# Kernel tuning notes

Measured on AMD Instinct MI355X. Metric: run time of the kernel, lower is better.

The kernel has to match this reference:

```python
import jax, jax.numpy as jnp
import numpy as np

EMBED_DIM = 768
NUM_HEADS = 12
HEAD_DIM = EMBED_DIM // NUM_HEADS
EPS = 1e-5  # nn.LayerNorm default


def setup_inputs() -> dict:
    key = jax.random.key(0)
    ks = jax.random.split(key, 7)
    D = EMBED_DIM
    s1 = 1.0 / np.sqrt(D)
    x = jax.random.normal(ks[0], (2, 2048, D), dtype=jnp.float32)
    # LayerNorm params
    gamma = jnp.ones((D,), jnp.float32)
    beta = jnp.zeros((D,), jnp.float32)
    # QKV projection (linear1): weight [3D, D], bias [3D]
    w1 = jax.random.uniform(ks[1], (3 * D, D), jnp.float32, -s1, s1)
    b1 = jax.random.uniform(ks[2], (3 * D,), jnp.float32, -s1, s1)
    # Output projection (linear2[0]): weight [D, D], bias [D]
    w2 = jax.random.uniform(ks[3], (D, D), jnp.float32, -s1, s1)
    b2 = jax.random.uniform(ks[4], (D,), jnp.float32, -s1, s1)
    return {"x": x, "gamma": gamma, "beta": beta, "w1": w1, "b1": b1, "w2": w2, "b2": b2}


def _layernorm(x, gamma, beta):
    mu = jnp.mean(x, axis=-1, keepdims=True)
    var = jnp.mean(jnp.square(x - mu), axis=-1, keepdims=True)
    return (x - mu) * jax.lax.rsqrt(var + EPS) * gamma + beta


def reference(x, gamma, beta, w1, b1, w2, b2) -> jnp.ndarray:
    B, L, D = x.shape
    H, Dh = NUM_HEADS, HEAD_DIM
    residual = x
    h = _layernorm(x, gamma, beta)
    qkv = h @ w1.T + b1  # [B, L, 3D]
    q, k, v = jnp.split(qkv, 3, axis=-1)
    # 'b n (h d) -> b h n d'
    q = q.reshape(B, L, H, Dh).transpose(0, 2, 1, 3)
    k = k.reshape(B, L, H, Dh).transpose(0, 2, 1, 3)
    v = v.reshape(B, L, H, Dh).transpose(0, 2, 1, 3)
    scores = jnp.einsum("bhqd,bhkd->bhqk", q, k) / jnp.sqrt(jnp.float32(Dh))
    attn = jax.nn.softmax(scores, axis=-1)  # dropout is identity in eval mode
    out = jnp.einsum("bhqk,bhkd->bhqd", attn, v)  # [B, H, L, Dh]
    out = out.transpose(0, 2, 1, 3).reshape(B, L, D)
    out = out @ w2.T + b2  # dropout identity in eval
    return residual + out
```

## Files before the change

kernel.cpp:

```cpp
#include <hip/hip_runtime.h>


#define DEV __device__ __forceinline__

typedef __attribute__((ext_vector_type(4))) float f32x4;
typedef __attribute__((ext_vector_type(8))) short s16x8;
typedef __attribute__((ext_vector_type(2))) int i32x2;

constexpr int Bb   = 2;
constexpr int Ll   = 2048;
constexpr int Dd   = 768;
constexpr int Hh   = 12;
constexpr int Dh   = 64;
constexpr int Mrows = Bb * Ll;
constexpr int N1   = 3 * Dd;

DEV unsigned short f2bf(float f) {
  union { float f; unsigned u; } v; v.f = f;
  unsigned r = v.u + 0x7fffu + ((v.u >> 16) & 1u);
  return (unsigned short)(r >> 16);
}

DEV void gload_lds16(const void* g, void* l) {
  __builtin_amdgcn_global_load_lds((const __attribute__((address_space(1))) unsigned int*)g,
                                   (__attribute__((address_space(3))) unsigned int*)l,
                                   16, 0, 0);
}

DEV f32x4 mfma16(s16x8 a, s16x8 b, f32x4 c) {
  return __builtin_amdgcn_mfma_f32_16x16x32_bf16(a, b, c, 0, 0, 0);
}

DEV float fexp2(float x) { float r; asm("v_exp_f32 %0, %1" : "=v"(r) : "v"(x)); return r; }
DEV float frcp(float x)  { float r; asm("v_rcp_f32 %0, %1" : "=v"(r) : "v"(x)); return r; }

DEV float redmax64(float x) {
  x = fmaxf(x, __shfl_xor(x, 16, 64));
  float a = x, b = x;
  asm volatile("v_permlane32_swap_b32 %0, %1" : "+v"(a), "+v"(b));
  return fmaxf(a, b);
}
DEV float redsum64(float x) {
  x += __shfl_xor(x, 16, 64);
  float a = x, b = x;
  asm volatile("v_permlane32_swap_b32 %0, %1" : "+v"(a), "+v"(b));
  return a + b;
}

DEV void ln_body(int row, int t, const float* __restrict__ x,
                 const float* __restrict__ gamma, const float* __restrict__ beta,
                 short* __restrict__ hbuf, float* red) {
  const float* xr = x + (size_t)row * Dd;
  float v0 = xr[t], v1 = xr[t + 256], v2 = xr[t + 512];
  float s = v0 + v1 + v2;
  float q = v0 * v0 + v1 * v1 + v2 * v2;
#pragma unroll
  for (int off = 32; off; off >>= 1) {
    s += __shfl_xor(s, off, 64);
    q += __shfl_xor(q, off, 64);
  }
  const int w = t >> 6, lane = t & 63;
  if (lane == 0) { red[w] = s; red[4 + w] = q; }
  __syncthreads();
  s = red[0] + red[1] + red[2] + red[3];
  q = red[4] + red[5] + red[6] + red[7];
  const float mean = s * (1.f / Dd);
  const float var  = q * (1.f / Dd) - mean * mean;
  const float rstd = rsqrtf(var + 1e-5f);
  short* hr = hbuf + (size_t)row * Dd;
  hr[t]       = (short)f2bf((v0 - mean) * rstd * gamma[t]       + beta[t]);
  hr[t + 256] = (short)f2bf((v1 - mean) * rstd * gamma[t + 256] + beta[t + 256]);
  hr[t + 512] = (short)f2bf((v2 - mean) * rstd * gamma[t + 512] + beta[t + 512]);
}

constexpr int W1E = N1 * Dd;
constexpr int W2E = Dd * Dd;

__global__ __launch_bounds__(256) void ln_kernel(const float* __restrict__ x,
                                                 const float* __restrict__ gamma,
                                                 const float* __restrict__ beta,
                                                 short* __restrict__ hbuf) {
  __shared__ float red[8];
  ln_body(blockIdx.x, threadIdx.x, x, gamma, beta, hbuf, red);
}

__global__ __launch_bounds__(256) void cvt_kernel(const float* __restrict__ w1,
                                                  const float* __restrict__ w2,
                                                  short* __restrict__ w1b,
                                                  short* __restrict__ w2b) {
  int i = blockIdx.x * 256 + threadIdx.x;
  const int stride = gridDim.x * 256;
  for (; i < W1E + W2E; i += stride) {
    if (i < W1E) w1b[i] = (short)f2bf(w1[i]);
    else         w2b[i - W1E] = (short)f2bf(w2[i - W1E]);
  }
}

__global__ __launch_bounds__(256) void prep_kernel(const float* __restrict__ x,
                                                   const float* __restrict__ gamma,
                                                   const float* __restrict__ beta,
                                                   short* __restrict__ hbuf,
                                                   const float* __restrict__ w1,
                                                   const float* __restrict__ w2,
                                                   short* __restrict__ w1b,
                                                   short* __restrict__ w2b) {
  __shared__ float red[8];
  if (blockIdx.x < (unsigned)Mrows) {
    ln_body(blockIdx.x, threadIdx.x, x, gamma, beta, hbuf, red);
  } else {
    int i = (blockIdx.x - Mrows) * 256 + threadIdx.x;
    for (; i < W1E + W2E; i += 1024 * 256) {
      if (i < W1E) w1b[i] = (short)f2bf(w1[i]);
      else         w2b[i - W1E] = (short)f2bf(w2[i - W1E]);
    }
  }
}

DEV unsigned xcd_swz(unsigned f, unsigned nwg) {
  if ((nwg & 7u) != 0u) return f;
  return (f & 7u) * (nwg >> 3) + (f >> 3);
}

template <int EPI, int WSRC>
__global__ __launch_bounds__(256) void gemm_bt(const short* __restrict__ A,
                                               const void* __restrict__ Wp,
                                               const float* __restrict__ bias,
                                               const float* __restrict__ resid,
                                               void* __restrict__ outp,
                                               int N, int K) {
  __shared__ __align__(16) short As[2][128 * 64];
  __shared__ __align__(16) short Ws[2][128 * 64];
  const int tid  = threadIdx.x;
  const int lane = tid & 63, wid = tid >> 6;
  const int wr = wid >> 1, wc = wid & 1;
  const int g = lane >> 4, li = lane & 15;
  const unsigned o = xcd_swz(blockIdx.y * gridDim.x + blockIdx.x,
                             gridDim.x * gridDim.y);
  const int brow = (int)(o / gridDim.x) * 128, bcol = (int)(o % gridDim.x) * 128;

  f32x4 acc[4][4];
#pragma unroll
  for (int m = 0; m < 4; ++m)
#pragma unroll
    for (int n = 0; n < 4; ++n)
#pragma unroll
      for (int r = 0; r < 4; ++r) acc[m][n][r] = 0.f;

  if constexpr (WSRC == 0) {
    const short* W = (const short*)Wp;
    const int nt = K >> 6;
    auto stage = [&](int t, int buf) {
      const int ko = t << 6;
#pragma unroll
      for (int i = 0; i < 4; ++i) {
        const int idx = i * 256 + tid;
        const int r = idx >> 3, c = idx & 7;
        const int cs = c ^ (r & 7);
        gload_lds16(A + (size_t)(brow + r) * K + ko + cs * 8,
                    (char*)&As[buf][0] + idx * 16);
        gload_lds16(W + (size_t)(bcol + r) * K + ko + cs * 8,
                    (char*)&Ws[buf][0] + idx * 16);
      }
    };
    stage(0, 0);
    stage(1, 1);
    for (int it = 0; it < nt; ++it) {
      const int cur = it & 1;
      if (it + 1 < nt) asm volatile("s_waitcnt vmcnt(8)" ::: "memory");
      else             asm volatile("s_waitcnt vmcnt(0)" ::: "memory");
      __builtin_amdgcn_s_barrier();
      __builtin_amdgcn_sched_barrier(0);
#pragma unroll
      for (int kk = 0; kk < 2; ++kk) {
        s16x8 af[4], bf[4];
#pragma unroll
        for (int m = 0; m < 4; ++m) {
          const int row = wr * 64 + m * 16 + li;
          af[m] = *(const s16x8*)&As[cur][row * 64 + (((kk * 4 + g) ^ (li & 7)) & 7) * 8];
        }
#pragma unroll
        for (int n = 0; n < 4; ++n) {
          const int row = wc * 64 + n * 16 + li;
          bf[n] = *(const s16x8*)&Ws[cur][row * 64 + (((kk * 4 + g) ^ (li & 7)) & 7) * 8];
        }
#pragma unroll
        for (int m = 0; m < 4; ++m)
#pragma unroll
          for (int n = 0; n < 4; ++n)
            acc[m][n] = mfma16(af[m], bf[n], acc[m][n]);
      }
      __builtin_amdgcn_s_barrier();
      if (it + 2 < nt) stage(it + 2, cur);
    }
  } else {
    const float* W = (const float*)Wp;
    for (int kt = 0; kt < K; kt += 64) {
#pragma unroll
      for (int i = 0; i < 4; ++i) {
        const int idx = i * 256 + tid;
        const int r = idx >> 3, c = idx & 7;
        const int cs = c ^ (r & 7);
        gload_lds16(A + (size_t)(brow + r) * K + kt + cs * 8,
                    (char*)&As[0][0] + idx * 16);
      }
#pragma unroll
      for (int i = 0; i < 4; ++i) {
        const int idx = i * 256 + tid;
        const int r = idx >> 3, c = idx & 7;
        const float* wp = W + (size_t)(bcol + r) * K + kt + c * 8;
        const f32x4 lo = *(const f32x4*)wp;
        const f32x4 hi = *(const f32x4*)(wp + 4);
        s16x8 oo;
#pragma unroll
        for (int j = 0; j < 4; ++j) {
          oo[j]     = (short)f2bf(lo[j]);
          oo[4 + j] = (short)f2bf(hi[j]);
        }
        *(s16x8*)((char*)&Ws[0][0] + (size_t)(r * 8 + (c ^ (r & 7))) * 16) = oo;
      }
      __syncthreads();
#pragma unroll
      for (int kk = 0; kk < 2; ++kk) {
        s16x8 af[4], bf[4];
#pragma unroll
        for (int m = 0; m < 4; ++m) {
          const int row = wr * 64 + m * 16 + li;
          af[m] = *(const s16x8*)&As[0][row * 64 + (((kk * 4 + g) ^ (li & 7)) & 7) * 8];
        }
#pragma unroll
        for (int n = 0; n < 4; ++n) {
          const int row = wc * 64 + n * 16 + li;
          bf[n] = *(const s16x8*)&Ws[0][row * 64 + (((kk * 4 + g) ^ (li & 7)) & 7) * 8];
        }
#pragma unroll
        for (int m = 0; m < 4; ++m)
#pragma unroll
          for (int n = 0; n < 4; ++n)
            acc[m][n] = mfma16(af[m], bf[n], acc[m][n]);
      }
      __syncthreads();
    }
  }

#pragma unroll
  for (int m = 0; m < 4; ++m) {
#pragma unroll
    for (int n = 0; n < 4; ++n) {
      const int col = bcol + wc * 64 + n * 16 + li;
      const float bv = bias[col];
#pragma unroll
      for (int r = 0; r < 4; ++r) {
        const int row = brow + wr * 64 + m * 16 + g * 4 + r;
        const float v = acc[m][n][r] + bv;
        if (EPI == 0) {
          ((short*)outp)[(size_t)row * N + col] = (short)f2bf(v);
        } else {
          const size_t o2 = (size_t)row * N + col;
          ((float*)outp)[o2] = v + resid[o2];
        }
      }
    }
  }
}

#define TRRD(dst, addr, OFF)                                                   \
  asm volatile("ds_read_b64_tr_b16 %0, %1 offset:" #OFF                        \
               : "=v"(dst) : "v"(addr))

__global__ __launch_bounds__(256) void attn_kernel(const short* __restrict__ qkv,
                                                   short* __restrict__ obuf) {
  __shared__ __align__(16) short Ks[2][64 * 64];
  __shared__ __align__(16) short Vt[2][64 * 64];
  __shared__ __align__(16) short Ps[4][16 * 64];
  const int tid  = threadIdx.x;
  const int lane = tid & 63, w = tid >> 6;
  const int g = lane >> 4, li = lane & 15;
  const unsigned o = xcd_swz(blockIdx.y * 32u + blockIdx.x, gridDim.x * gridDim.y);
  const int bh = (int)(o >> 5);
  const int b = bh / Hh, h = bh % Hh;
  const size_t rowbase = (size_t)b * Ll * N1;
  const int q0 = (int)(o & 31u) * 64 + w * 16;
  constexpr float kScale = 0.125f * 1.44269504f;
  constexpr float kThrRaw = 8.f / kScale;
  constexpr int KVSTRIDE = 64 * N1;

  s16x8 qf[2];
#pragma unroll
  for (int ks = 0; ks < 2; ++ks)
    qf[ks] = *(const s16x8*)(qkv + rowbase + (size_t)(q0 + li) * N1 +
                             h * Dh + ks * 32 + g * 8);

  f32x4 oa[4];
  float m_ = -1e30f, l_ = 0.f;
#pragma unroll
  for (int dn = 0; dn < 4; ++dn)
#pragma unroll
    for (int r = 0; r < 4; ++r) oa[dn][r] = 0.f;

  constexpr int NT = Ll / 64;

  const int ia = tid, ib = 256 + tid;
  const int ra = ia >> 3, ca = ia & 7, rb = ib >> 3, cb = ib & 7;
  const short* kpa = qkv + rowbase + Dd + h * Dh + (size_t)ra * N1 + (ca ^ (ra & 7)) * 8;
  const short* kpb = qkv + rowbase + Dd + h * Dh + (size_t)rb * N1 + (cb ^ (rb & 7)) * 8;
  const int Ta = ia >> 3, Tb = ib >> 3;
  const short* vpa = qkv + rowbase + 2 * Dd + h * Dh +
                     (size_t)((Ta & 15) * 4 + (ca >> 1)) * N1 + (Ta >> 4) * 16 + (ia & 1) * 8;
  const short* vpb = qkv + rowbase + 2 * Dd + h * Dh +
                     (size_t)((Tb & 15) * 4 + (cb >> 1)) * N1 + (Tb >> 4) * 16 + (ib & 1) * 8;
  char* KsB = (char*)&Ks[0][0];
  char* VtB = (char*)&Vt[0][0];
  const int dsta = ia * 16, dstb = ib * 16;

  int koff[4][2];
#pragma unroll
  for (int n = 0; n < 4; ++n) {
    koff[n][0] = ((n * 16 + li) * 64 + ((g ^ (li & 7)) & 7) * 8) * 2;
    koff[n][1] = ((n * 16 + li) * 64 + (((4 + g) ^ (li & 7)) & 7) * 8) * 2;
  }
  int pwoff[4], proff[2];
#pragma unroll
  for (int n = 0; n < 4; ++n)
    pwoff[n] = li * 128 + (((2 * n + (g >> 1)) ^ (li & 7)) << 4) + 8 * (g & 1);
#pragma unroll
  for (int kk = 0; kk < 2; ++kk)
    proff[kk] = li * 128 + (((4 * kk + g) ^ (li & 7)) << 4);
  char* Pw = (char*)&Ps[w][0];
  const unsigned vlane = (unsigned)((lane >> 4) * 256 + (lane & 15) * 2);
  const unsigned vbase0 = (unsigned)(unsigned long long)(&Vt[0][0]) + vlane;

  auto stageK = [&](int buf) {
    const int bo = buf << 13;
    gload_lds16(kpa, KsB + bo + dsta);
    gload_lds16(kpb, KsB + bo + dstb);
    kpa += KVSTRIDE; kpb += KVSTRIDE;
  };
  auto stageV = [&](int buf) {
    const int bo = buf << 13;
    gload_lds16(vpa, VtB + bo + dsta);
    gload_lds16(vpb, VtB + bo + dstb);
    vpa += KVSTRIDE; vpb += KVSTRIDE;
  };

  stageK(0); stageV(0); stageK(1); stageV(1);
  asm volatile("s_waitcnt vmcnt(4)" ::: "memory");
  __builtin_amdgcn_s_barrier();
  __builtin_amdgcn_sched_barrier(0);

  f32x4 zA[4], zB[4];
#pragma unroll
  for (int n = 0; n < 4; ++n) {
    s16x8 kf0 = *(const s16x8*)(KsB + koff[n][0]);
    s16x8 kf1 = *(const s16x8*)(KsB + koff[n][1]);
    f32x4 z;
#pragma unroll
    for (int r = 0; r < 4; ++r) z[r] = 0.f;
    z = mfma16(kf0, qf[0], z);
    z = mfma16(kf1, qf[1], z);
    zA[n] = z;
  }

  for (int kt = 0; kt < NT; ++kt) {
    const int cur = kt & 1;
    const int curo = cur << 13;
    const int nxto = (cur ^ 1) << 13;
    if (kt + 1 < NT) asm volatile("s_waitcnt vmcnt(2)" ::: "memory");
    else             asm volatile("s_waitcnt vmcnt(0)" ::: "memory");
    __builtin_amdgcn_s_barrier();
    __builtin_amdgcn_sched_barrier(0);

    if (kt + 2 < NT) stageK(cur);

    if (kt + 1 < NT) {
      __builtin_amdgcn_s_setprio(1);
#pragma unroll
      for (int n = 0; n < 4; ++n) {
        s16x8 kf0 = *(const s16x8*)(KsB + nxto + koff[n][0]);
        s16x8 kf1 = *(const s16x8*)(KsB + nxto + koff[n][1]);
        f32x4 z;
#pragma unroll
        for (int r = 0; r < 4; ++r) z[r] = 0.f;
        z = mfma16(kf0, qf[0], z);
        z = mfma16(kf1, qf[1], z);
        zB[n] = z;
      }
      __builtin_amdgcn_s_setprio(0);
    }

    const float l0 = fmaxf(fmaxf(zA[0][0], zA[0][1]), zA[0][2]);
    const float l1 = fmaxf(fmaxf(zA[0][3], zA[1][0]), zA[1][1]);
    const float l2 = fmaxf(fmaxf(zA[1][2], zA[1][3]), zA[2][0]);
    const float l3 = fmaxf(fmaxf(zA[2][1], zA[2][2]), zA[2][3]);
    const float l4 = fmaxf(fmaxf(zA[3][0], zA[3][1]), zA[3][2]);
    float mx = fmaxf(fmaxf(fmaxf(fmaxf(l0, l1), l2), fmaxf(l3, l4)), zA[3][3]);
    mx = redmax64(mx);
    if (!__all(mx - m_ <= kThrRaw)) {
      const float mnew = fmaxf(m_, mx);
      const float sc = fexp2((m_ - mnew) * kScale);
      float scq[4];
#pragma unroll
      for (int r = 0; r < 4; ++r)
        scq[r] = __shfl(sc, (lane & 48) + ((lane & 48) >> 2) + r, 64);
#pragma unroll
      for (int dn = 0; dn < 4; ++dn)
#pragma unroll
        for (int r = 0; r < 4; ++r) oa[dn][r] *= scq[r];
      l_ *= sc;
      m_ = mnew;
    }
    const float msc = m_ * kScale;
    float rs = 0.f;
#pragma unroll
    for (int n = 0; n < 4; ++n)
#pragma unroll
      for (int r = 0; r < 4; ++r) {
        const float p = fexp2(fmaf(zA[n][r], kScale, -msc));
        zA[n][r] = p;
        rs += p;
      }
    rs = redsum64(rs);
    l_ += rs;

#pragma unroll
    for (int n = 0; n < 4; ++n) {
      unsigned u0, u1;
      asm("v_cvt_pk_bf16_f32 %0, %1, %2" : "=v"(u0) : "v"(zA[n][0]), "v"(zA[n][1]));
      asm("v_cvt_pk_bf16_f32 %0, %1, %2" : "=v"(u1) : "v"(zA[n][2]), "v"(zA[n][3]));
      i32x2 pv; pv[0] = (int)u0; pv[1] = (int)u1;
      *(i32x2*)(Pw + pwoff[n]) = pv;
    }

    s16x8 pf[2];
#pragma unroll
    for (int kk = 0; kk < 2; ++kk)
      pf[kk] = *(const s16x8*)(Pw + proff[kk]);

    union VU { long l[2]; s16x8 v; };
    VU vu[4][2];
    {
      const unsigned vaddr = vbase0 + (unsigned)curo;
      TRRD(vu[0][0].l[0], vaddr, 0);    TRRD(vu[0][0].l[1], vaddr, 128);
      TRRD(vu[0][1].l[0], vaddr, 1024); TRRD(vu[0][1].l[1], vaddr, 1152);
      TRRD(vu[1][0].l[0], vaddr, 2048); TRRD(vu[1][0].l[1], vaddr, 2176);
      TRRD(vu[1][1].l[0], vaddr, 3072); TRRD(vu[1][1].l[1], vaddr, 3200);
      TRRD(vu[2][0].l[0], vaddr, 4096); TRRD(vu[2][0].l[1], vaddr, 4224);
      TRRD(vu[2][1].l[0], vaddr, 5120); TRRD(vu[2][1].l[1], vaddr, 5248);
      TRRD(vu[3][0].l[0], vaddr, 6144); TRRD(vu[3][0].l[1], vaddr, 6272);
      TRRD(vu[3][1].l[0], vaddr, 7168); TRRD(vu[3][1].l[1], vaddr, 7296);
    }
    asm volatile("s_waitcnt lgkmcnt(0)" ::: "memory");
    __builtin_amdgcn_sched_barrier(0);

    __builtin_amdgcn_s_setprio(1);
#pragma unroll
    for (int dn = 0; dn < 4; ++dn) {
      oa[dn] = mfma16(pf[0], vu[dn][0].v, oa[dn]);
      oa[dn] = mfma16(pf[1], vu[dn][1].v, oa[dn]);
    }
    __builtin_amdgcn_s_setprio(0);

    __builtin_amdgcn_s_barrier();
    if (kt + 2 < NT) stageV(cur);
    if (kt + 1 < NT) {
#pragma unroll
      for (int n = 0; n < 4; ++n) zA[n] = zB[n];
    }
  }

  {
#pragma unroll
    for (int r = 0; r < 4; ++r) {
      const float lq = __shfl(l_, (lane & 48) + ((lane & 48) >> 2) + r, 64);
      const float inv = frcp(lq);
      const int row = b * Ll + q0 + g * 4 + r;
#pragma unroll
      for (int dn = 0; dn < 4; ++dn)
        obuf[(size_t)row * Dd + h * Dh + dn * 16 + li] =
            (short)f2bf(oa[dn][r] * inv);
    }
  }
}

extern "C" void kernel_launch(void* const* d_in, const int* in_sizes, int n_in,
                              void* d_out, int out_size, void* d_ws, size_t ws_size,
                              hipStream_t stream) {
  const float* x     = (const float*)d_in[0];
  const float* gamma = (const float*)d_in[1];
  const float* beta  = (const float*)d_in[2];
  const float* w1    = (const float*)d_in[3];
  const float* b1    = (const float*)d_in[4];
  const float* w2    = (const float*)d_in[5];
  const float* b2    = (const float*)d_in[6];
  float* out = (float*)d_out;
  char* ws = (char*)d_ws;

  if (ws_size >= 29884416) {
    short* qkvb = (short*)(ws);
    short* hb   = (short*)(ws + 18874368);
    short* w1b  = (short*)(ws + 25165824);
    short* w2b  = (short*)(ws + 28704768);
    prep_kernel<<<dim3(Mrows + 1024), dim3(256), 0, stream>>>(
        x, gamma, beta, hb, w1, w2, w1b, w2b);
    gemm_bt<0, 0><<<dim3(N1 / 128, Mrows / 128), dim3(256), 0, stream>>>(
        hb, w1b, b1, nullptr, (void*)qkvb, N1, Dd);
    attn_kernel<<<dim3(Ll / 64, Bb * Hh), dim3(256), 0, stream>>>(qkvb, hb);
    gemm_bt<1, 0><<<dim3(Dd / 128, Mrows / 128), dim3(256), 0, stream>>>(
        hb, w2b, b2, x, (void*)out, Dd, Dd);
  } else if (ws_size >= 17301504) {
    short* qkvb = (short*)(ws);
    short* hb   = (short*)(ws + 9437184);
    short* w1b  = (short*)(ws + 12582912);
    short* w2b  = (short*)(ws + 16121856);
    cvt_kernel<<<dim3(1024), dim3(256), 0, stream>>>(w1, w2, w1b, w2b);
    for (int b = 0; b < Bb; ++b) {
      const size_t ro = (size_t)b * Ll * Dd;
      ln_kernel<<<dim3(Ll), dim3(256), 0, stream>>>(x + ro, gamma, beta, hb);
      gemm_bt<0, 0><<<dim3(N1 / 128, Ll / 128), dim3(256), 0, stream>>>(
          hb, w1b, b1, nullptr, (void*)qkvb, N1, Dd);
      attn_kernel<<<dim3(Ll / 64, Hh), dim3(256), 0, stream>>>(qkvb, hb);
      gemm_bt<1, 0><<<dim3(Dd / 128, Ll / 128), dim3(256), 0, stream>>>(
          hb, w2b, b2, x + ro, (void*)(out + ro), Dd, Dd);
    }
  } else {
    short* qkvb = (short*)(ws);
    short* hb   = (short*)(ws + 9437184);
    for (int b = 0; b < Bb; ++b) {
      const size_t ro = (size_t)b * Ll * Dd;
      ln_kernel<<<dim3(Ll), dim3(256), 0, stream>>>(x + ro, gamma, beta, hb);
      gemm_bt<0, 1><<<dim3(N1 / 128, Ll / 128), dim3(256), 0, stream>>>(
          hb, w1, b1, nullptr, (void*)qkvb, N1, Dd);
      attn_kernel<<<dim3(Ll / 64, Hh), dim3(256), 0, stream>>>(qkvb, hb);
      gemm_bt<1, 1><<<dim3(Dd / 128, Ll / 128), dim3(256), 0, stream>>>(
          hb, w2, b2, x + ro, (void*)(out + ro), Dd, Dd);
    }
  }
}
```

Measured before the change: 114.2 us.

## Rewrite attention with 32x32 MFMA, register-resident P and split-KV wave pairs

The attention kernel now uses 32x32x16 bf16 MFMAs. Each wave handles 32 query rows, and the two wave pairs each process half of the KV sequence (16 tiles each), with a final LDS merge of the partial softmax states. P is converted and rearranged in registers with permlane32 swaps instead of a round-trip through LDS. The old double-buffered K/V prefetch pipeline and the early QK^T overlap are dropped in favour of a simple load, wait and compute loop per tile, which risks exposing global load latency.

Result: slower. 122.2 us (+7.0%).

```diff
diff --git a/kernel.cpp b/kernel.cpp
--- a/kernel.cpp
+++ b/kernel.cpp
@@ -4,6 +4,7 @@
 #define DEV __device__ __forceinline__
 
 typedef __attribute__((ext_vector_type(4))) float f32x4;
+typedef __attribute__((ext_vector_type(16))) float f32x16;
 typedef __attribute__((ext_vector_type(8))) short s16x8;
 typedef __attribute__((ext_vector_type(2))) int i32x2;
 
@@ -30,22 +31,12 @@
 DEV f32x4 mfma16(s16x8 a, s16x8 b, f32x4 c) {
   return __builtin_amdgcn_mfma_f32_16x16x32_bf16(a, b, c, 0, 0, 0);
 }
+DEV f32x16 mfma32(s16x8 a, s16x8 b, f32x16 c) {
+  return __builtin_amdgcn_mfma_f32_32x32x16_bf16(a, b, c, 0, 0, 0);
+}
 
 DEV float fexp2(float x) { float r; asm("v_exp_f32 %0, %1" : "=v"(r) : "v"(x)); return r; }
 DEV float frcp(float x)  { float r; asm("v_rcp_f32 %0, %1" : "=v"(r) : "v"(x)); return r; }
-
-DEV float redmax64(float x) {
-  x = fmaxf(x, __shfl_xor(x, 16, 64));
-  float a = x, b = x;
-  asm volatile("v_permlane32_swap_b32 %0, %1" : "+v"(a), "+v"(b));
-  return fmaxf(a, b);
-}
-DEV float redsum64(float x) {
-  x += __shfl_xor(x, 16, 64);
-  float a = x, b = x;
-  asm volatile("v_permlane32_swap_b32 %0, %1" : "+v"(a), "+v"(b));
-  return a + b;
-}
 
 DEV void ln_body(int row, int t, const float* __restrict__ x,
                  const float* __restrict__ gamma, const float* __restrict__ beta,
@@ -271,213 +262,207 @@
                                                    short* __restrict__ obuf) {
   __shared__ __align__(16) short Ks[2][64 * 64];
   __shared__ __align__(16) short Vt[2][64 * 64];
-  __shared__ __align__(16) short Ps[4][16 * 64];
   const int tid  = threadIdx.x;
   const int lane = tid & 63, w = tid >> 6;
-  const int g = lane >> 4, li = lane & 15;
+  const int pair = w >> 1, qh = w & 1;
+  const int l5 = lane >> 5, lq = lane & 31;
   const unsigned o = xcd_swz(blockIdx.y * 32u + blockIdx.x, gridDim.x * gridDim.y);
   const int bh = (int)(o >> 5);
   const int b = bh / Hh, h = bh % Hh;
   const size_t rowbase = (size_t)b * Ll * N1;
-  const int q0 = (int)(o & 31u) * 64 + w * 16;
+  const int q0 = (int)(o & 31u) * 64 + qh * 32;
   constexpr float kScale = 0.125f * 1.44269504f;
   constexpr float kThrRaw = 8.f / kScale;
-  constexpr int KVSTRIDE = 64 * N1;
-
-  s16x8 qf[2];
-#pragma unroll
-  for (int ks = 0; ks < 2; ++ks)
-    qf[ks] = *(const s16x8*)(qkv + rowbase + (size_t)(q0 + li) * N1 +
-                             h * Dh + ks * 32 + g * 8);
-
-  f32x4 oa[4];
+  constexpr int KVS = 64 * N1;
+  constexpr int NT = 16;
+
+  s16x8 qf[4];
+#pragma unroll
+  for (int mf = 0; mf < 4; ++mf)
+    qf[mf] = *(const s16x8*)(qkv + rowbase + (size_t)(q0 + lq) * N1 +
+                             h * Dh + mf * 16 + l5 * 8);
+
+  f32x16 oa[2];
+#pragma unroll
+  for (int rt = 0; rt < 2; ++rt)
+#pragma unroll
+    for (int i = 0; i < 16; ++i) oa[rt][i] = 0.f;
   float m_ = -1e30f, l_ = 0.f;
-#pragma unroll
-  for (int dn = 0; dn < 4; ++dn)
-#pragma unroll
-    for (int r = 0; r < 4; ++r) oa[dn][r] = 0.f;
-
-  constexpr int NT = Ll / 64;
-
-  const int ia = tid, ib = 256 + tid;
-  const int ra = ia >> 3, ca = ia & 7, rb = ib >> 3, cb = ib & 7;
-  const short* kpa = qkv + rowbase + Dd + h * Dh + (size_t)ra * N1 + (ca ^ (ra & 7)) * 8;
-  const short* kpb = qkv + rowbase + Dd + h * Dh + (size_t)rb * N1 + (cb ^ (rb & 7)) * 8;
-  const int Ta = ia >> 3, Tb = ib >> 3;
-  const short* vpa = qkv + rowbase + 2 * Dd + h * Dh +
-                     (size_t)((Ta & 15) * 4 + (ca >> 1)) * N1 + (Ta >> 4) * 16 + (ia & 1) * 8;
-  const short* vpb = qkv + rowbase + 2 * Dd + h * Dh +
-                     (size_t)((Tb & 15) * 4 + (cb >> 1)) * N1 + (Tb >> 4) * 16 + (ib & 1) * 8;
-  char* KsB = (char*)&Ks[0][0];
-  char* VtB = (char*)&Vt[0][0];
-  const int dsta = ia * 16, dstb = ib * 16;
-
-  int koff[4][2];
-#pragma unroll
-  for (int n = 0; n < 4; ++n) {
-    koff[n][0] = ((n * 16 + li) * 64 + ((g ^ (li & 7)) & 7) * 8) * 2;
-    koff[n][1] = ((n * 16 + li) * 64 + (((4 + g) ^ (li & 7)) & 7) * 8) * 2;
-  }
-  int pwoff[4], proff[2];
-#pragma unroll
-  for (int n = 0; n < 4; ++n)
-    pwoff[n] = li * 128 + (((2 * n + (g >> 1)) ^ (li & 7)) << 4) + 8 * (g & 1);
-#pragma unroll
-  for (int kk = 0; kk < 2; ++kk)
-    proff[kk] = li * 128 + (((4 * kk + g) ^ (li & 7)) << 4);
-  char* Pw = (char*)&Ps[w][0];
-  const unsigned vlane = (unsigned)((lane >> 4) * 256 + (lane & 15) * 2);
-  const unsigned vbase0 = (unsigned)(unsigned long long)(&Vt[0][0]) + vlane;
-
-  auto stageK = [&](int buf) {
-    const int bo = buf << 13;
-    gload_lds16(kpa, KsB + bo + dsta);
-    gload_lds16(kpb, KsB + bo + dstb);
-    kpa += KVSTRIDE; kpb += KVSTRIDE;
-  };
-  auto stageV = [&](int buf) {
-    const int bo = buf << 13;
-    gload_lds16(vpa, VtB + bo + dsta);
-    gload_lds16(vpb, VtB + bo + dstb);
-    vpa += KVSTRIDE; vpb += KVSTRIDE;
-  };
-
-  stageK(0); stageV(0); stageK(1); stageV(1);
-  asm volatile("s_waitcnt vmcnt(4)" ::: "memory");
-  __builtin_amdgcn_s_barrier();
-  __builtin_amdgcn_sched_barrier(0);
-
-  f32x4 zA[4], zB[4];
-#pragma unroll
-  for (int n = 0; n < 4; ++n) {
-    s16x8 kf0 = *(const s16x8*)(KsB + koff[n][0]);
-    s16x8 kf1 = *(const s16x8*)(KsB + koff[n][1]);
-    f32x4 z;
-#pragma unroll
-    for (int r = 0; r < 4; ++r) z[r] = 0.f;
-    z = mfma16(kf0, qf[0], z);
-    z = mfma16(kf1, qf[1], z);
-    zA[n] = z;
-  }
+
+  const short* gp[8];
+  char* dp[8];
+#pragma unroll
+  for (int i = 0; i < 8; ++i) {
+    const int ii = (i & 1) * 256 + tid;
+    const int p = i >> 2;
+    if (((i >> 1) & 1) == 0) {
+      const int r = ii >> 3, c = ii & 7;
+      gp[i] = qkv + rowbase + (size_t)(p * 1024 + r) * N1 + Dd + h * Dh + (c ^ (r & 7)) * 8;
+      dp[i] = (char*)&Ks[p][0] + ii * 16;
+    } else {
+      const int T = ii >> 3;
+      const int kv = (T & 15) * 4 + ((ii & 7) >> 1);
+      const int d0 = (T >> 4) * 16 + (ii & 1) * 8;
+      gp[i] = qkv + rowbase + (size_t)(p * 1024 + kv) * N1 + 2 * Dd + h * Dh + d0;
+      dp[i] = (char*)&Vt[p][0] + ii * 16;
+    }
+  }
+
+  int koff[2][4];
+#pragma unroll
+  for (int rt = 0; rt < 2; ++rt)
+#pragma unroll
+    for (int mf = 0; mf < 4; ++mf) {
+      const int r = rt * 32 + lq;
+      koff[rt][mf] = (r * 8 + ((2 * mf + l5) ^ (r & 7))) * 16;
+    }
+  char* pK = (char*)&Ks[pair][0];
+  const unsigned vbase = (unsigned)(unsigned long long)(&Vt[pair][0]) +
+                         (unsigned)(((lane >> 4) & 1) * 2048 + l5 * 256 + (lane & 15) * 2);
 
   for (int kt = 0; kt < NT; ++kt) {
-    const int cur = kt & 1;
-    const int curo = cur << 13;
-    const int nxto = (cur ^ 1) << 13;
-    if (kt + 1 < NT) asm volatile("s_waitcnt vmcnt(2)" ::: "memory");
-    else             asm volatile("s_waitcnt vmcnt(0)" ::: "memory");
+#pragma unroll
+    for (int i = 0; i < 8; ++i) { gload_lds16(gp[i], dp[i]); gp[i] += KVS; }
+    asm volatile("s_waitcnt vmcnt(0)" ::: "memory");
     __builtin_amdgcn_s_barrier();
     __builtin_amdgcn_sched_barrier(0);
 
-    if (kt + 2 < NT) stageK(cur);
-
-    if (kt + 1 < NT) {
-      __builtin_amdgcn_s_setprio(1);
-#pragma unroll
-      for (int n = 0; n < 4; ++n) {
-        s16x8 kf0 = *(const s16x8*)(KsB + nxto + koff[n][0]);
-        s16x8 kf1 = *(const s16x8*)(KsB + nxto + koff[n][1]);
-        f32x4 z;
-#pragma unroll
-        for (int r = 0; r < 4; ++r) z[r] = 0.f;
-        z = mfma16(kf0, qf[0], z);
-        z = mfma16(kf1, qf[1], z);
-        zB[n] = z;
-      }
-      __builtin_amdgcn_s_setprio(0);
-    }
-
-    const float l0 = fmaxf(fmaxf(zA[0][0], zA[0][1]), zA[0][2]);
-    const float l1 = fmaxf(fmaxf(zA[0][3], zA[1][0]), zA[1][1]);
-    const float l2 = fmaxf(fmaxf(zA[1][2], zA[1][3]), zA[2][0]);
-    const float l3 = fmaxf(fmaxf(zA[2][1], zA[2][2]), zA[2][3]);
-    const float l4 = fmaxf(fmaxf(zA[3][0], zA[3][1]), zA[3][2]);
-    float mx = fmaxf(fmaxf(fmaxf(fmaxf(l0, l1), l2), fmaxf(l3, l4)), zA[3][3]);
-    mx = redmax64(mx);
+    f32x16 z[2];
+    __builtin_amdgcn_s_setprio(1);
+#pragma unroll
+    for (int rt = 0; rt < 2; ++rt) {
+      f32x16 zz;
+#pragma unroll
+      for (int i = 0; i < 16; ++i) zz[i] = 0.f;
+#pragma unroll
+      for (int mf = 0; mf < 4; ++mf) {
+        s16x8 kf = *(const s16x8*)(pK + koff[rt][mf]);
+        zz = mfma32(kf, qf[mf], zz);
+      }
+      z[rt] = zz;
+    }
+    __builtin_amdgcn_s_setprio(0);
+
+    float t16[16];
+#pragma unroll
+    for (int i = 0; i < 16; ++i) t16[i] = fmaxf(z[0][i], z[1][i]);
+#pragma unroll
+    for (int st = 8; st; st >>= 1)
+#pragma unroll
+      for (int i = 0; i < st; ++i) t16[i] = fmaxf(t16[i], t16[i + st]);
+    float mx = t16[0];
+    { float a2 = mx, b2 = mx;
+      asm volatile("v_permlane32_swap_b32 %0, %1" : "+v"(a2), "+v"(b2));
+      mx = fmaxf(a2, b2); }
     if (!__all(mx - m_ <= kThrRaw)) {
       const float mnew = fmaxf(m_, mx);
       const float sc = fexp2((m_ - mnew) * kScale);
-      float scq[4];
-#pragma unroll
-      for (int r = 0; r < 4; ++r)
-        scq[r] = __shfl(sc, (lane & 48) + ((lane & 48) >> 2) + r, 64);
-#pragma unroll
-      for (int dn = 0; dn < 4; ++dn)
-#pragma unroll
-        for (int r = 0; r < 4; ++r) oa[dn][r] *= scq[r];
+#pragma unroll
+      for (int rt = 0; rt < 2; ++rt)
+#pragma unroll
+        for (int i = 0; i < 16; ++i) oa[rt][i] *= sc;
       l_ *= sc;
       m_ = mnew;
     }
     const float msc = m_ * kScale;
     float rs = 0.f;
 #pragma unroll
-    for (int n = 0; n < 4; ++n)
-#pragma unroll
-      for (int r = 0; r < 4; ++r) {
-        const float p = fexp2(fmaf(zA[n][r], kScale, -msc));
-        zA[n][r] = p;
+    for (int rt = 0; rt < 2; ++rt)
+#pragma unroll
+      for (int i = 0; i < 16; ++i) {
+        const float p = fexp2(fmaf(z[rt][i], kScale, -msc));
+        z[rt][i] = p;
         rs += p;
       }
-    rs = redsum64(rs);
+    { float a2 = rs, b2 = rs;
+      asm volatile("v_permlane32_swap_b32 %0, %1" : "+v"(a2), "+v"(b2));
+      rs = a2 + b2; }
     l_ += rs;
 
-#pragma unroll
-    for (int n = 0; n < 4; ++n) {
-      unsigned u0, u1;
-      asm("v_cvt_pk_bf16_f32 %0, %1, %2" : "=v"(u0) : "v"(zA[n][0]), "v"(zA[n][1]));
-      asm("v_cvt_pk_bf16_f32 %0, %1, %2" : "=v"(u1) : "v"(zA[n][2]), "v"(zA[n][3]));
-      i32x2 pv; pv[0] = (int)u0; pv[1] = (int)u1;
-      *(i32x2*)(Pw + pwoff[n]) = pv;
-    }
-
-    s16x8 pf[2];
-#pragma unroll
-    for (int kk = 0; kk < 2; ++kk)
-      pf[kk] = *(const s16x8*)(Pw + proff[kk]);
-
-    union VU { long l[2]; s16x8 v; };
-    VU vu[4][2];
-    {
-      const unsigned vaddr = vbase0 + (unsigned)curo;
-      TRRD(vu[0][0].l[0], vaddr, 0);    TRRD(vu[0][0].l[1], vaddr, 128);
-      TRRD(vu[0][1].l[0], vaddr, 1024); TRRD(vu[0][1].l[1], vaddr, 1152);
-      TRRD(vu[1][0].l[0], vaddr, 2048); TRRD(vu[1][0].l[1], vaddr, 2176);
-      TRRD(vu[1][1].l[0], vaddr, 3072); TRRD(vu[1][1].l[1], vaddr, 3200);
-      TRRD(vu[2][0].l[0], vaddr, 4096); TRRD(vu[2][0].l[1], vaddr, 4224);
-      TRRD(vu[2][1].l[0], vaddr, 5120); TRRD(vu[2][1].l[1], vaddr, 5248);
-      TRRD(vu[3][0].l[0], vaddr, 6144); TRRD(vu[3][0].l[1], vaddr, 6272);
-      TRRD(vu[3][1].l[0], vaddr, 7168); TRRD(vu[3][1].l[1], vaddr, 7296);
-    }
+    unsigned plo[2][4], phi[2][4];
+#pragma unroll
+    for (int rt = 0; rt < 2; ++rt)
+#pragma unroll
+      for (int i2 = 0; i2 < 4; ++i2) {
+        asm("v_cvt_pk_bf16_f32 %0, %1, %2"
+            : "=v"(plo[rt][i2]) : "v"(z[rt][4 * i2 + 0]), "v"(z[rt][4 * i2 + 1]));
+        asm("v_cvt_pk_bf16_f32 %0, %1, %2"
+            : "=v"(phi[rt][i2]) : "v"(z[rt][4 * i2 + 2]), "v"(z[rt][4 * i2 + 3]));
+      }
+    union PF { unsigned u[4]; s16x8 v; } pf[4];
+#pragma unroll
+    for (int mf = 0; mf < 4; ++mf) {
+      const int t = mf >> 1, j2 = mf & 1;
+      unsigned s0 = plo[t][2 * j2], d0 = plo[t][2 * j2 + 1];
+      asm volatile("v_permlane32_swap_b32 %0, %1" : "+v"(d0), "+v"(s0));
+      unsigned s1 = phi[t][2 * j2], d1 = phi[t][2 * j2 + 1];
+      asm volatile("v_permlane32_swap_b32 %0, %1" : "+v"(d1), "+v"(s1));
+      pf[mf].u[0] = s0; pf[mf].u[1] = s1; pf[mf].u[2] = d0; pf[mf].u[3] = d1;
+    }
+
+    union VU { long l[2]; s16x8 v; } vu[2][4];
+    TRRD(vu[0][0].l[0], vbase, 0);    TRRD(vu[0][0].l[1], vbase, 128);
+    TRRD(vu[0][1].l[0], vbase, 512);  TRRD(vu[0][1].l[1], vbase, 640);
+    TRRD(vu[0][2].l[0], vbase, 1024); TRRD(vu[0][2].l[1], vbase, 1152);
+    TRRD(vu[0][3].l[0], vbase, 1536); TRRD(vu[0][3].l[1], vbase, 1664);
+    TRRD(vu[1][0].l[0], vbase, 4096); TRRD(vu[1][0].l[1], vbase, 4224);
+    TRRD(vu[1][1].l[0], vbase, 4608); TRRD(vu[1][1].l[1], vbase, 4736);
+    TRRD(vu[1][2].l[0], vbase, 5120); TRRD(vu[1][2].l[1], vbase, 5248);
+    TRRD(vu[1][3].l[0], vbase, 5632); TRRD(vu[1][3].l[1], vbase, 5760);
     asm volatile("s_waitcnt lgkmcnt(0)" ::: "memory");
     __builtin_amdgcn_sched_barrier(0);
 
     __builtin_amdgcn_s_setprio(1);
 #pragma unroll
-    for (int dn = 0; dn < 4; ++dn) {
-      oa[dn] = mfma16(pf[0], vu[dn][0].v, oa[dn]);
-      oa[dn] = mfma16(pf[1], vu[dn][1].v, oa[dn]);
-    }
+    for (int dt = 0; dt < 2; ++dt)
+#pragma unroll
+      for (int kvmf = 0; kvmf < 4; ++kvmf)
+        oa[dt] = mfma32(vu[dt][kvmf].v, pf[kvmf].v, oa[dt]);
     __builtin_amdgcn_s_setprio(0);
 
     __builtin_amdgcn_s_barrier();
-    if (kt + 2 < NT) stageV(cur);
-    if (kt + 1 < NT) {
-#pragma unroll
-      for (int n = 0; n < 4; ++n) zA[n] = zB[n];
-    }
-  }
-
-  {
-#pragma unroll
-    for (int r = 0; r < 4; ++r) {
-      const float lq = __shfl(l_, (lane & 48) + ((lane & 48) >> 2) + r, 64);
-      const float inv = frcp(lq);
-      const int row = b * Ll + q0 + g * 4 + r;
-#pragma unroll
-      for (int dn = 0; dn < 4; ++dn)
-        obuf[(size_t)row * Dd + h * Dh + dn * 16 + li] =
-            (short)f2bf(oa[dn][r] * inv);
-    }
+  }
+
+  if (pair == 0) {
+    char* ob = (char*)&Ks[0][0] + qh * 8192;
+#pragma unroll
+    for (int rt = 0; rt < 2; ++rt)
+#pragma unroll
+      for (int i = 0; i < 16; ++i)
+        *(float*)(ob + ((rt * 16 + i) << 8) + (lane << 2)) = oa[rt][i];
+    char* mb = (char*)&Vt[0][0] + qh * 512 + lq * 8;
+    *(float*)mb = m_;
+    *(float*)(mb + 4) = l_;
+  }
+  __syncthreads();
+  if (pair == 1) {
+    char* ob = (char*)&Ks[0][0] + qh * 8192;
+    char* mb = (char*)&Vt[0][0] + qh * 512 + lq * 8;
+    const float m0 = *(float*)mb, l0 = *(float*)(mb + 4);
+    const float mm = fmaxf(m_, m0);
+    const float s1 = fexp2((m_ - mm) * kScale);
+    const float s0 = fexp2((m0 - mm) * kScale);
+    const float inv = frcp(l_ * s1 + l0 * s0);
+    short* op = obuf + (size_t)(b * Ll + q0 + lq) * Dd + h * Dh;
+#pragma unroll
+    for (int rt = 0; rt < 2; ++rt)
+#pragma unroll
+      for (int i2 = 0; i2 < 4; ++i2) {
+        float v0_, v1_, v2_, v3_;
+        {
+          const int i = 4 * i2;
+          v0_ = (oa[rt][i + 0] * s1 + *(float*)(ob + ((rt * 16 + i + 0) << 8) + (lane << 2)) * s0) * inv;
+          v1_ = (oa[rt][i + 1] * s1 + *(float*)(ob + ((rt * 16 + i + 1) << 8) + (lane << 2)) * s0) * inv;
+          v2_ = (oa[rt][i + 2] * s1 + *(float*)(ob + ((rt * 16 + i + 2) << 8) + (lane << 2)) * s0) * inv;
+          v3_ = (oa[rt][i + 3] * s1 + *(float*)(ob + ((rt * 16 + i + 3) << 8) + (lane << 2)) * s0) * inv;
+        }
+        unsigned u01, u23;
+        asm("v_cvt_pk_bf16_f32 %0, %1, %2" : "=v"(u01) : "v"(v0_), "v"(v1_));
+        asm("v_cvt_pk_bf16_f32 %0, %1, %2" : "=v"(u23) : "v"(v2_), "v"(v3_));
+        const int d = rt * 32 + 8 * i2 + 4 * l5;
+        *(unsigned*)(op + d) = u01;
+        *(unsigned*)(op + d + 2) = u23;
+      }
   }
 }
 
```
